# Optimization experiments

Hardware: AMD Instinct MI355X
Metric: run time of the kernel (lower is better)

Reference implementation:

```python
import jax, jax.numpy as jnp
import numpy as np

SAMPLES = 1024
LAM = 0.00051
IOR = 1.515
T_PROP = 8.74
CA = 0.9
LENSLET_CA = 0.165
RMIN = 5.5 * (IOR - 1.0)
RMAX = 29.0 * (IOR - 1.0)
NZ = 10
NLENS = 29
TAU = 30.0
LSE_P = 0.01
PS = 3.6 / SAMPLES
K = 2.0 * np.pi / LAM


def _grids():
    xg = np.linspace(-1.8, 1.8, SAMPLES).astype(np.float32)
    xgm, ygm = np.meshgrid(xg, xg)
    fx = np.linspace(-1.0 / (2.0 * PS), 1.0 / (2.0 * PS), SAMPLES).astype(np.float32)
    Fx, Fy = np.meshgrid(fx, fx)
    return xgm, ygm, Fx, Fy


def _bessj1(x):
    # Numerical Recipes rational approximation of J1 (numpy, setup-time only)
    ax = np.abs(x)
    y = x * x
    p1 = x * (72362614232.0 + y * (-7895059235.0 + y * (242396853.1 + y * (-2972611.439 + y * (15704.48260 + y * (-30.16036606))))))
    q1 = 144725228442.0 + y * (2300535178.0 + y * (18583304.74 + y * (99447.43394 + y * (376.9991397 + y))))
    small = p1 / q1
    axs = np.maximum(ax, 1e-12)
    z = 8.0 / axs
    y2 = z * z
    xx = axs - 2.356194491
    p2 = 1.0 + y2 * (0.183105e-2 + y2 * (-0.3516396496e-4 + y2 * (0.2457520174e-5 + y2 * (-0.240337019e-6))))
    q2 = 0.04687499995 + y2 * (-0.2002690873e-3 + y2 * (0.8449199096e-5 + y2 * (-0.88228987e-6 + y2 * 0.105787412e-6)))
    big = np.sqrt(0.636619772 / axs) * (np.cos(xx) * p2 - z * np.sin(xx) * q2) * np.sign(x)
    return np.where(ax < 8.0, small, big)


def _target_and_mask():
    xgm, ygm, _, _ = _grids()
    target_res = 0.005 * 6  # target_res * M
    D = 1.22 * LAM / np.sin(2.0 * np.arctan(target_res / (2.0 * T_PROP)))
    xa = K * D * np.sin(np.arctan(xgm / T_PROP)) / 2.0
    ya = K * D * np.sin(np.arctan(ygm / T_PROP)) / 2.0
    Ra = np.sqrt(xa * xa + ya * ya)
    ta = (2.0 * _bessj1(Ra) / Ra) ** 2
    ta = ta / np.sqrt(np.sum(ta ** 2))
    tF = np.abs(np.fft.fft2(np.fft.fftshift(ta))) ** 2
    dcm = np.ones_like(tF)
    dcm[:3, :3] = 0; dcm[-2:, :1] = 0; dcm[:1, -2:] = 0; dcm[-2:, -2:] = 0
    dc_mask = ((dcm * tF) > 1e-3 * tF.max()).astype(np.float32)
    return tF.astype(np.float32), dc_mask


def setup_inputs() -> dict:
    rng = np.random.default_rng(0)
    rlist = rng.permutation(1.0 / np.linspace(1.0 / RMAX, 1.0 / RMIN, NLENS)).astype(np.float32)
    th = rng.uniform(0.0, 2.0 * np.pi, NLENS)
    rad = (CA - LENSLET_CA) * np.sqrt(rng.uniform(0.0, 1.0, NLENS))
    xpos = (rad * np.cos(th)).astype(np.float32)
    ypos = (rad * np.sin(th)).astype(np.float32)
    zmin_v = 1.0 / (1.0 / T_PROP - 1.0 / 5.5)
    zmax_v = 1.0 / (1.0 / T_PROP - 1.0 / 29.0)
    defocus = (1.0 / np.linspace(1.0 / zmin_v, 1.0 / zmax_v, NZ)).astype(np.float32)
    tF, dc_mask = _target_and_mask()
    return {
        'rlist': jnp.asarray(rlist), 'xpos': jnp.asarray(xpos), 'ypos': jnp.asarray(ypos),
        'defocus_list': jnp.asarray(defocus),
        'target_F': jnp.asarray(tF), 'dc_mask': jnp.asarray(dc_mask),
    }


def reference(rlist, xpos, ypos, defocus_list, target_F, dc_mask):
    xgm_np, ygm_np, Fx_np, Fy_np = _grids()
    xgm, ygm = jnp.asarray(xgm_np), jnp.asarray(ygm_np)
    Fx, Fy = jnp.asarray(Fx_np), jnp.asarray(Fy_np)

    # ---- lenslet surface synthesis (irregular per-lenslet scatter) ----
    dx2 = (xgm[None] - xpos[:, None, None]) ** 2 + (ygm[None] - ypos[:, None, None]) ** 2  # [N,H,W]
    in_lens = dx2 <= LENSLET_CA ** 2
    r = rlist[:, None, None]
    r2_safe = jnp.where(in_lens, dx2, 0.0)  # avoid nan grads outside lenslet
    sag = r - jnp.sqrt(jnp.maximum(r * r - r2_safe, 1e-12))  # plano-convex sag
    Tsurf = jnp.sum(jnp.where(in_lens, sag, 0.0), axis=0)  # [H,W]
    aper = ((jnp.sum(in_lens.astype(jnp.float32), axis=0) > 0) & (xgm ** 2 + ygm ** 2 <= CA ** 2)).astype(jnp.float32)
    phi_lens = (K * (IOR - 1.0)) * Tsurf

    # ---- angular-spectrum propagation kernel over distance t ----
    kz = jnp.sqrt(jnp.maximum((1.0 / LAM) ** 2 - Fx ** 2 - Fy ** 2, 0.0))
    H = jnp.fft.ifftshift(jnp.exp(1j * (2.0 * np.pi * T_PROP) * kz))

    def psf_one(z):
        phi_in = K * (xgm ** 2 + ygm ** 2) / (2.0 * z)  # paraxial defocus from virtual plane z
        U1 = aper * jnp.exp(1j * (phi_in + phi_lens))
        U2 = jnp.fft.ifft2(jnp.fft.fft2(U1) * H)
        p = jnp.abs(U2) ** 2
        return p / jnp.sum(p)  # l1 psf normalization

    zstack = jax.vmap(psf_one)(defocus_list)  # [Nz,H,W]

    # ---- stack spectrum ----
    S = jnp.fft.fft2(jnp.fft.fftshift(zstack, axes=(-2, -1)))  # [Nz,H,W] complex
    normsize = float(SAMPLES * SAMPLES)

    # diagonal terms: |S|^2 vs target autocorrelation spectrum, dc-masked
    diag = jnp.sum(dc_mask[None] * jnp.square((jnp.abs(S) ** 2 - target_F[None]) / normsize), axis=(-2, -1))  # [Nz]

    # off-diagonal terms: log-sum-exp of |cross-correlation|
    i1, i2 = np.triu_indices(NZ, k=1)  # 45 fixed pairs
    Fcorr = jnp.conj(S[i1]) * S[i2]  # [45,H,W]
    ccorr = jnp.abs(jnp.fft.ifft2(Fcorr))
    off = (TAU * LSE_P) * jax.scipy.special.logsumexp(ccorr.reshape(len(i1), -1) / LSE_P, axis=-1)  # [45]

    return jnp.concatenate([diag, off], axis=0)  # [55]
```

## Files before the change

kernel.cpp:

```cpp
#include <hip/hip_runtime.h>
#include <math.h>

#define NZ 10
#define NLENS 29
#define NPAIR 45
#define NUNIT 23

static __device__ __forceinline__ float2 cmulf(float2 a, float2 b){
    return make_float2(a.x*b.x - a.y*b.y, a.x*b.y + a.y*b.x);
}
#define SW(i) ((i) ^ (((i)>>5)&31))
#define WB() __builtin_amdgcn_wave_barrier()

static constexpr double PI2   = 6.283185307179586;
static constexpr double KD    = PI2/0.00051;
static constexpr double F0D   = 1.0/(2.0*(3.6/1024.0));
static constexpr double FSTEP = 2.0*F0D/1023.0;
static constexpr double IL2D  = (1.0/0.00051)*(1.0/0.00051);
static constexpr double TPPID = PI2*8.74;

static __device__ __forceinline__ void load_W(float2* W, const float2* Wg, int tid){
    for (int t = tid; t < 1024; t += 256) W[SW(t)] = Wg[t];
}

template<bool INV>
static __device__ __forceinline__ void bf4(const float2 a[4], float2 w1, float2 w2, float2 w3, float2 o[4]){
    if (INV){ w1.y = -w1.y; w2.y = -w2.y; w3.y = -w3.y; }
    float2 a1 = cmulf(a[1], w1), a2 = cmulf(a[2], w2), a3 = cmulf(a[3], w3);
    float2 t0 = make_float2(a[0].x+a2.x, a[0].y+a2.y);
    float2 t1 = make_float2(a[0].x-a2.x, a[0].y-a2.y);
    float2 t2 = make_float2(a1.x+a3.x, a1.y+a3.y);
    float2 t3 = make_float2(a1.x-a3.x, a1.y-a3.y);
    o[0] = make_float2(t0.x+t2.x, t0.y+t2.y);
    o[2] = make_float2(t0.x-t2.x, t0.y-t2.y);
    if (!INV){
        o[1] = make_float2(t1.x + t3.y, t1.y - t3.x);
        o[3] = make_float2(t1.x - t3.y, t1.y + t3.x);
    } else {
        o[1] = make_float2(t1.x - t3.y, t1.y + t3.x);
        o[3] = make_float2(t1.x + t3.y, t1.y - t3.x);
    }
}
template<bool INV>
static __device__ __forceinline__ void bf4nt(const float2 a[4], float2 o[4]){
    float2 t0 = make_float2(a[0].x+a[2].x, a[0].y+a[2].y);
    float2 t1 = make_float2(a[0].x-a[2].x, a[0].y-a[2].y);
    float2 t2 = make_float2(a[1].x+a[3].x, a[1].y+a[3].y);
    float2 t3 = make_float2(a[1].x-a[3].x, a[1].y-a[3].y);
    o[0] = make_float2(t0.x+t2.x, t0.y+t2.y);
    o[2] = make_float2(t0.x-t2.x, t0.y-t2.y);
    if (!INV){
        o[1] = make_float2(t1.x + t3.y, t1.y - t3.x);
        o[3] = make_float2(t1.x - t3.y, t1.y + t3.x);
    } else {
        o[1] = make_float2(t1.x - t3.y, t1.y + t3.x);
        o[3] = make_float2(t1.x + t3.y, t1.y - t3.x);
    }
}

static __device__ __forceinline__ void r16_load(const float2* B, int t, float2 a[4][4]){
    #pragma unroll
    for (int k = 0; k < 4; ++k)
        #pragma unroll
        for (int q = 0; q < 4; ++q)
            a[k][q] = B[SW(t + 64*k + 256*q)];
}
template<bool INV>
static __device__ __forceinline__ void r16_s14(const float2 a[4][4], const float2* W, float2 z[4][4]){
    float2 y[4][4];
    #pragma unroll
    for (int k = 0; k < 4; ++k) bf4nt<INV>(a[k], y[k]);
    #pragma unroll
    for (int i = 0; i < 4; ++i){
        float2 b[4] = { y[0][i], y[1][i], y[2][i], y[3][i] };
        bf4<INV>(b, W[SW(64*i)], W[SW(128*i)], W[SW(192*i)], z[i]);
    }
}
static __device__ __forceinline__ void r16_st1(float2* B, int t, const float2 z[4][4]){
    #pragma unroll
    for (int i = 0; i < 4; ++i)
        #pragma unroll
        for (int d = 0; d < 4; ++d)
            B[SW(16*t + i + 4*d)] = z[i][d];
}
template<bool INV>
static __device__ __forceinline__ void r16_s16_64(const float2 a[4][4], const float2* W, int t, float2 z[4][4]){
    int mt = t & 15;
    float2 y[4][4];
    float2 w1 = W[SW(16*mt)], w2 = W[SW(32*mt)], w3 = W[SW(48*mt)];
    #pragma unroll
    for (int k = 0; k < 4; ++k) bf4<INV>(a[k], w1, w2, w3, y[k]);
    #pragma unroll
    for (int n = 0; n < 4; ++n){
        int m2 = mt + 16*n;
        float2 b[4] = { y[0][n], y[1][n], y[2][n], y[3][n] };
        bf4<INV>(b, W[SW(4*m2)], W[SW(8*m2)], W[SW(12*m2)], z[n]);
    }
}
static __device__ __forceinline__ void r16_st2(float2* B, int t, const float2 z[4][4]){
    int base = 256*(t>>4) + (t&15);
    #pragma unroll
    for (int n = 0; n < 4; ++n)
        #pragma unroll
        for (int d = 0; d < 4; ++d)
            B[SW(base + 16*n + 64*d)] = z[n][d];
}
template<bool INV>
static __device__ __forceinline__ void r16_s256(const float2 a[4][4], const float2* W, int t, float2 z[4][4]){
    #pragma unroll
    for (int k = 0; k < 4; ++k){
        int j = t + 64*k;
        bf4<INV>(a[k], W[SW(j)], W[SW(2*j)], W[SW(3*j)], z[k]);
    }
}
static __device__ __forceinline__ void r16_st3(float2* B, int t, const float2 z[4][4]){
    #pragma unroll
    for (int k = 0; k < 4; ++k)
        #pragma unroll
        for (int d = 0; d < 4; ++d)
            B[SW(t + 64*k + 256*d)] = z[k][d];
}
template<bool INV>
static __device__ void r16_fft_regs(float2* B, const float2* W, int t, float2 a[4][4], float2 z[4][4]){
    float2 b[4][4];
    r16_s14<INV>(a, W, z);
    WB(); r16_st1(B, t, z); WB();
    r16_load(B, t, b); r16_s16_64<INV>(b, W, t, z);
    WB(); r16_st2(B, t, z); WB();
    r16_load(B, t, b); r16_s256<INV>(b, W, t, z);
}
template<bool INV>
static __device__ void r16_fft_lds(float2* B, const float2* W, int t, float2 z[4][4]){
    float2 a[4][4];
    r16_load(B, t, a);
    r16_fft_regs<INV>(B, W, t, a, z);
}

static __device__ __forceinline__ float2 expi_from_double(double ph){
    double t = ph * (1.0/PI2);
    t -= floor(t);
    float th = (float)(t * PI2);
    float s, c; sincosf(th, &s, &c);
    return make_float2(c, s);
}

__global__ __launch_bounds__(256) void k_prep(const float* __restrict__ rlist,
        const float* __restrict__ xpos, const float* __restrict__ ypos,
        const float* __restrict__ tF, const float* __restrict__ dm,
        float2* __restrict__ phiA, float2* __restrict__ HT,
        float2* __restrict__ TM, float2* __restrict__ Wg){
    __shared__ float2 T[32][33];
    int b = blockIdx.x, tid = threadIdx.x;
    if (b < 4096){
        int idx = b*256 + tid;
        int r = idx >> 10, c = idx & 1023;
        float x = (float)(-1.8 + c*(3.6/1023.0));
        float y = (float)(-1.8 + r*(3.6/1023.0));
        const float ca2 = (float)(0.165*0.165);
        float Ts = 0.f; int any = 0;
        for (int l = 0; l < NLENS; ++l){
            float dx = x - xpos[l], dy = y - ypos[l];
            float d2 = dx*dx + dy*dy;
            if (d2 <= ca2){
                float rr = rlist[l];
                Ts += rr - sqrtf(fmaxf(rr*rr - d2, 1e-12f));
                any = 1;
            }
        }
        float ap = (any && (x*x + y*y) <= 0.81f) ? 1.f : 0.f;
        float phi = (float)(KD*(1.515 - 1.0)) * Ts;
        phiA[idx] = make_float2(phi, ap);
    } else if (b < 8192){
        int idx = (b-4096)*256 + tid;
        int c = idx >> 10, r = idx & 1023;
        int cs = (c + 512) & 1023, rs = (r + 512) & 1023;
        float fc = (float)(-F0D + cs*FSTEP);
        float fr = (float)(-F0D + rs*FSTEP);
        float kz2 = __fsub_rn(__fsub_rn((float)IL2D, __fmul_rn(fc,fc)), __fmul_rn(fr,fr));
        float kzf = sqrtf(fmaxf(kz2, 0.f));
        float phf = __fmul_rn((float)TPPID, kzf);
        HT[idx] = expi_from_double((double)phf);
    } else if (b < 9216){
        int tb = b - 8192;
        int bx = tb & 31, by = tb >> 5;
        int tx = tid & 31, ty = tid >> 5;
        #pragma unroll
        for (int j = 0; j < 4; ++j){
            int r = by*32 + ty + 8*j, c = bx*32 + tx;
            T[ty+8*j][tx] = make_float2(tF[(size_t)r*1024 + c], dm[(size_t)r*1024 + c]);
        }
        __syncthreads();
        #pragma unroll
        for (int j = 0; j < 4; ++j){
            int c = bx*32 + ty + 8*j, r = by*32 + tx;
            TM[(size_t)c*1024 + r] = T[tx][ty+8*j];
        }
    } else {
        int t = (b-9216)*256 + tid;
        float a = (float)((double)t * (-PI2/1024.0));
        float s, c; sincosf(a, &s, &c);
        Wg[t] = make_float2(c, s);
    }
}

__global__ __launch_bounds__(256) void k_p1(const float2* __restrict__ phiA,
        const float* __restrict__ defocus, float2* __restrict__ S,
        const float2* __restrict__ Wg){
    __shared__ float2 buf[4*1024];
    __shared__ float2 W[1024];
    int tid = threadIdx.x, zz = blockIdx.y;
    load_W(W, Wg, tid);
    __syncthreads();
    int w = tid >> 6, t = tid & 63;
    int row = blockIdx.x*4 + w;
    float2* B = buf + w*1024;
    float zf = defocus[zz];
    float y  = (float)(-1.8 + row*(3.6/1023.0));
    const float KF = (float)KD;
    const float2* pha = phiA + ((size_t)row << 10);
    float2 a[4][4], z[4][4];
    #pragma unroll
    for (int k = 0; k < 4; ++k)
        #pragma unroll
        for (int q = 0; q < 4; ++q){
            int idx = t + 64*k + 256*q;
            float x = (float)(-1.8 + idx*(3.6/1023.0));
            float2 pa = pha[idx];
            float2 u  = make_float2(0.f, 0.f);
            if (pa.y != 0.f){
                float qq     = x*x + y*y;
                float phi_in = (KF*qq) / (2.0f*zf);
                u = expi_from_double((double)(phi_in + pa.x));
            }
            a[k][q] = u;
        }
    r16_fft_regs<false>(B, W, t, a, z);
    float2* Srow = S + ((size_t)zz << 20) + ((size_t)row << 10);
    #pragma unroll
    for (int k = 0; k < 4; ++k)
        #pragma unroll
        for (int d = 0; d < 4; ++d)
            Srow[t + 64*k + 256*d] = z[k][d];
}

__global__ __launch_bounds__(256) void k_p2(float2* __restrict__ S,
        const float2* __restrict__ HT, const float2* __restrict__ Wg){
    __shared__ float2 buf[4*1024];
    __shared__ float2 W[1024];
    int tid = threadIdx.x, bx = blockIdx.x, zz = blockIdx.y;
    int cb = ((bx & 7) << 5) | (bx >> 3);
    int c0 = cb*4;
    load_W(W, Wg, tid);
    float2* Sz = S + ((size_t)zz << 20);
    for (int it = 0; it < 16; ++it){
        int rr = it*64 + (tid>>2), cc = tid & 3;
        buf[cc*1024 + SW(rr)] = Sz[((size_t)rr << 10) + c0 + cc];
    }
    __syncthreads();
    int col = tid >> 6, t = tid & 63;
    float2* B = buf + col*1024;
    float2 z[4][4], a[4][4];
    r16_fft_lds<false>(B, W, t, z);
    const float2* Hc = HT + ((size_t)(c0+col) << 10);
    #pragma unroll
    for (int k = 0; k < 4; ++k)
        #pragma unroll
        for (int d = 0; d < 4; ++d)
            z[k][d] = cmulf(z[k][d], Hc[t + 64*k + 256*d]);
    r16_fft_regs<true>(B, W, t, z, a);
    const float sc = 1.0f/1024.0f;
    #pragma unroll
    for (int k = 0; k < 4; ++k)
        #pragma unroll
        for (int d = 0; d < 4; ++d){ a[k][d].x *= sc; a[k][d].y *= sc; }
    WB();
    r16_st3(B, t, a);
    __syncthreads();
    for (int it = 0; it < 16; ++it){
        int rr = it*64 + (tid>>2), cc = tid & 3;
        Sz[((size_t)rr << 10) + c0 + cc] = buf[cc*1024 + SW(rr)];
    }
}

__global__ __launch_bounds__(256) void k_p3(float2* __restrict__ S,
        float* __restrict__ sumPart, const float2* __restrict__ Wg){
    __shared__ float2 buf[4*1024];
    __shared__ float2 W[1024];
    int tid = threadIdx.x, zz = blockIdx.y;
    load_W(W, Wg, tid);
    __syncthreads();
    int w = tid >> 6, t = tid & 63;
    int row = blockIdx.x*4 + w;
    float2* B = buf + w*1024;
    float2* Srow = S + ((size_t)zz << 20) + ((size_t)row << 10);
    float2 a[4][4], z[4][4];
    #pragma unroll
    for (int k = 0; k < 4; ++k)
        #pragma unroll
        for (int q = 0; q < 4; ++q)
            a[k][q] = Srow[t + 64*k + 256*q];
    r16_fft_regs<true>(B, W, t, a, z);
    const float s2 = (1.0f/1024.0f)*(1.0f/1024.0f);
    float lsum = 0.f;
    #pragma unroll
    for (int k = 0; k < 4; ++k)
        #pragma unroll
        for (int d = 0; d < 4; ++d){
            float2 u = z[k][d];
            float p = (u.x*u.x + u.y*u.y) * s2;
            a[k][d] = make_float2(p, 0.f);
            lsum += p;
        }
    for (int o = 32; o > 0; o >>= 1) lsum += __shfl_down(lsum, o, 64);
    if (t == 0) sumPart[zz*1024 + row] = lsum;
    WB();
    r16_fft_regs<false>(B, W, t, a, z);
    #pragma unroll
    for (int k = 0; k < 4; ++k)
        #pragma unroll
        for (int d = 0; d < 4; ++d)
            Srow[t + 64*k + 256*d] = z[k][d];
}

__global__ __launch_bounds__(256) void k_p4(float2* __restrict__ S,
        const float* __restrict__ sumPart, const float2* __restrict__ TM,
        float* __restrict__ dpart, const float2* __restrict__ Wg){
    __shared__ float2 buf[4*1024];
    __shared__ float2 W[1024];
    int tid = threadIdx.x, bx = blockIdx.x, zz = blockIdx.y;
    int cb = ((bx & 7) << 5) | (bx >> 3);
    int c0 = cb*4;
    load_W(W, Wg, tid);
    float2* Sz = S + ((size_t)zz << 20);
    for (int it = 0; it < 16; ++it){
        int rr = it*64 + (tid>>2), cc = tid & 3;
        buf[cc*1024 + SW(rr)] = Sz[((size_t)rr << 10) + c0 + cc];
    }
    int col = tid >> 6, t = tid & 63;
    double sd = 0.0;
    for (int i = t; i < 1024; i += 64) sd += (double)sumPart[zz*1024 + i];
    for (int o = 32; o > 0; o >>= 1) sd += __shfl_down(sd, o, 64);
    sd = __shfl(sd, 0, 64);
    float inv = (float)(1.0/sd);
    __syncthreads();
    float2* B = buf + col*1024;
    float2 z[4][4];
    r16_fft_lds<false>(B, W, t, z);
    const float2* TMc = TM + ((size_t)(c0+col) << 10);
    const float nrm = 1.0f/1048576.0f;
    float dacc = 0.f;
    #pragma unroll
    for (int k = 0; k < 4; ++k)
        #pragma unroll
        for (int d = 0; d < 4; ++d){
            float2 s = z[k][d]; s.x *= inv; s.y *= inv; z[k][d] = s;
            float2 tm = TMc[t + 64*k + 256*d];
            float dff = (s.x*s.x + s.y*s.y - tm.x) * nrm;
            dacc += tm.y * dff * dff;
        }
    for (int o = 32; o > 0; o >>= 1) dacc += __shfl_down(dacc, o, 64);
    WB();
    r16_st3(B, t, z);
    __syncthreads();
    if (t == 0) ((float*)W)[col] = dacc;
    for (int it = 0; it < 16; ++it){
        int rr = it*64 + (tid>>2), cc = tid & 3;
        Sz[((size_t)rr << 10) + c0 + cc] = buf[cc*1024 + SW(rr)];
    }
    __syncthreads();
    if (tid == 0){
        float* r = (float*)W;
        dpart[zz*256 + cb] = r[0]+r[1]+r[2]+r[3];
    }
}

static __device__ __forceinline__ void pair_of(int p, int& a, int& b){
    int i = 0, c = NZ-1;
    while (p >= c){ p -= c; ++i; --c; }
    a = i; b = i + 1 + p;
}

__global__ __launch_bounds__(256) void k_pairA(const float2* __restrict__ S,
        float2* __restrict__ U, int ubase, const float2* __restrict__ Wg){
    __shared__ float2 buf[4*1024];
    __shared__ float2 W[1024];
    int tid = threadIdx.x, ug = blockIdx.y;
    load_W(W, Wg, tid);
    __syncthreads();
    int w = tid >> 6, t = tid & 63;
    int row = blockIdx.x*4 + w;
    float2* B = buf + w*1024;
    int u = ubase + ug;
    int pa = 2*u, pb = (2*u+1 < NPAIR) ? (2*u+1) : (NPAIR-1);
    int i1, i2, j1, j2;
    pair_of(pa, i1, i2); pair_of(pb, j1, j2);
    const float2* A1 = S + ((size_t)i1 << 20) + ((size_t)row << 10);
    const float2* A2 = S + ((size_t)i2 << 20) + ((size_t)row << 10);
    const float2* B1 = S + ((size_t)j1 << 20) + ((size_t)row << 10);
    const float2* B2 = S + ((size_t)j2 << 20) + ((size_t)row << 10);
    float2 a[4][4], z[4][4];
    #pragma unroll
    for (int k = 0; k < 4; ++k)
        #pragma unroll
        for (int q = 0; q < 4; ++q){
            int idx = t + 64*k + 256*q;
            float2 x1 = A1[idx], y1 = A2[idx], x2 = B1[idx], y2 = B2[idx];
            float2 g1 = make_float2(x1.x*y1.x + x1.y*y1.y, x1.x*y1.y - x1.y*y1.x);
            float2 g2 = make_float2(x2.x*y2.x + x2.y*y2.y, x2.x*y2.y - x2.y*y2.x);
            a[k][q] = make_float2(g1.x - g2.y, g1.y + g2.x);
        }
    r16_fft_regs<true>(B, W, t, a, z);
    const float sc = 1.0f/1024.0f;
    float2* Up = U + ((size_t)ug << 20) + ((size_t)row << 10);
    #pragma unroll
    for (int k = 0; k < 4; ++k)
        #pragma unroll
        for (int d = 0; d < 4; ++d){
            float2 v = z[k][d];
            Up[t + 64*k + 256*d] = make_float2(v.x*sc, v.y*sc);
        }
}

__global__ __launch_bounds__(256) void k_pairB(const float2* __restrict__ U,
        float2* __restrict__ lsePart, int ubase, const float2* __restrict__ Wg){
    __shared__ float2 buf[4*1024];
    __shared__ float2 W[1024];
    int tid = threadIdx.x, bx = blockIdx.x, ug = blockIdx.y;
    int cb = ((bx & 7) << 5) | (bx >> 3);
    int c0 = cb*4;
    int u = ubase + ug;
    load_W(W, Wg, tid);
    const float2* Up = U + ((size_t)ug << 20);
    for (int it = 0; it < 16; ++it){
        int rr = it*64 + (tid>>2), cc = tid & 3;
        buf[cc*1024 + SW(rr)] = Up[((size_t)rr << 10) + c0 + cc];
    }
    __syncthreads();
    int col = tid >> 6, t = tid & 63;
    float2* B = buf + col*1024;
    float2 z[4][4];
    r16_fft_lds<true>(B, W, t, z);
    const float sc = 1.0f/1024.0f;
    float m1 = -1.f, m2 = -1.f;
    #pragma unroll
    for (int k = 0; k < 4; ++k)
        #pragma unroll
        for (int d = 0; d < 4; ++d){
            float c1 = fabsf(z[k][d].x)*sc, c2 = fabsf(z[k][d].y)*sc;
            z[k][d] = make_float2(c1, c2);
            m1 = fmaxf(m1, c1); m2 = fmaxf(m2, c2);
        }
    for (int o = 32; o > 0; o >>= 1){
        m1 = fmaxf(m1, __shfl_down(m1, o, 64));
        m2 = fmaxf(m2, __shfl_down(m2, o, 64));
    }
    if (t == 0) B[0] = make_float2(m1, m2);
    __syncthreads();
    float M1 = -1.f, M2 = -1.f;
    #pragma unroll
    for (int ww = 0; ww < 4; ++ww){
        float2 v = buf[ww*1024];
        M1 = fmaxf(M1, v.x); M2 = fmaxf(M2, v.y);
    }
    float s1 = 0.f, s2 = 0.f;
    #pragma unroll
    for (int k = 0; k < 4; ++k)
        #pragma unroll
        for (int d = 0; d < 4; ++d){
            s1 += expf((z[k][d].x - M1) * 100.0f);
            s2 += expf((z[k][d].y - M2) * 100.0f);
        }
    for (int o = 32; o > 0; o >>= 1){
        s1 += __shfl_down(s1, o, 64);
        s2 += __shfl_down(s2, o, 64);
    }
    if (t == 0) B[1] = make_float2(s1, s2);
    __syncthreads();
    if (tid == 0){
        float S1 = 0.f, S2 = 0.f;
        #pragma unroll
        for (int ww = 0; ww < 4; ++ww){
            float2 v = buf[ww*1024 + 1];
            S1 += v.x; S2 += v.y;
        }
        lsePart[(size_t)(2*u)*256 + cb] = make_float2(M1, S1);
        if (2*u+1 < NPAIR)
            lsePart[(size_t)(2*u+1)*256 + cb] = make_float2(M2, S2);
    }
}

__global__ __launch_bounds__(256) void k_final(const float* __restrict__ dpart,
        const float2* __restrict__ lsePart, float* __restrict__ out){
    __shared__ double dred[4];
    __shared__ float fred[4];
    int b = blockIdx.x, tid = threadIdx.x;
    if (b < NZ){
        double s = (double)dpart[b*256 + tid];
        for (int o = 32; o > 0; o >>= 1) s += __shfl_down(s, o, 64);
        if ((tid & 63) == 0) dred[tid >> 6] = s;
        __syncthreads();
        if (tid == 0) out[b] = (float)(dred[0]+dred[1]+dred[2]+dred[3]);
    } else {
        int p = b - NZ;
        float2 v = lsePart[(size_t)p*256 + tid];
        float m = v.x;
        for (int o = 32; o > 0; o >>= 1) m = fmaxf(m, __shfl_down(m, o, 64));
        if ((tid & 63) == 0) fred[tid >> 6] = m;
        __syncthreads();
        float M = fmaxf(fmaxf(fred[0], fred[1]), fmaxf(fred[2], fred[3]));
        double s = (double)v.y * (double)expf((v.x - M)*100.0f);
        for (int o = 32; o > 0; o >>= 1) s += __shfl_down(s, o, 64);
        if ((tid & 63) == 0) dred[tid >> 6] = s;
        __syncthreads();
        if (tid == 0)
            out[NZ + p] = (float)(30.0*(double)M + 0.3*log(dred[0]+dred[1]+dred[2]+dred[3]));
    }
}

extern "C" void kernel_launch(void* const* d_in, const int* in_sizes, int n_in,
                              void* d_out, int out_size, void* d_ws, size_t ws_size,
                              hipStream_t stream){
    const float* rlist   = (const float*)d_in[0];
    const float* xpos    = (const float*)d_in[1];
    const float* ypos    = (const float*)d_in[2];
    const float* defocus = (const float*)d_in[3];
    const float* tF      = (const float*)d_in[4];
    const float* dmask   = (const float*)d_in[5];
    float* out = (float*)d_out;

    char* ws = (char*)d_ws;
    const size_t S_B = 83886080ull;
    float2* S       = (float2*)(ws);
    char*   tail    = ws + S_B;
    float*  sumPart = (float*) (tail);
    float*  dpart   = (float*) (tail + 65536);
    float2* lsePart = (float2*)(tail + 131072);
    float2* Wg      = (float2*)(tail + 229376);
    char*   X       = ws + S_B + 262144;
    float2* phiA    = (float2*)(X);
    float2* HT      = (float2*)(X + 8388608);
    float2* TM      = (float2*)(X + 16777216);
    float2* U       = (float2*)(X);

    size_t Xoff = S_B + 262144;
    int UB = (ws_size >= Xoff + (64ull<<20)) ? 8 : 6;

    k_prep<<<9220, 256, 0, stream>>>(rlist, xpos, ypos, tF, dmask, phiA, HT, TM, Wg);
    k_p1 <<<dim3(256, NZ), 256, 0, stream>>>(phiA, defocus, S, Wg);
    k_p2 <<<dim3(256, NZ), 256, 0, stream>>>(S, HT, Wg);
    k_p3 <<<dim3(256, NZ), 256, 0, stream>>>(S, sumPart, Wg);
    k_p4 <<<dim3(256, NZ), 256, 0, stream>>>(S, sumPart, TM, dpart, Wg);
    for (int g = 0; g < NUNIT; g += UB){
        int cnt = (NUNIT - g < UB) ? (NUNIT - g) : UB;
        k_pairA<<<dim3(256, cnt), 256, 0, stream>>>(S, U, g, Wg);
        k_pairB<<<dim3(256, cnt), 256, 0, stream>>>(U, lsePart, g, Wg);
    }
    k_final<<<NZ + NPAIR, 256, 0, stream>>>(dpart, lsePart, out);
}
```

Baseline: 525.4 us.

## Transpose FFT intermediates via LDS exchange, exploit Hermitian symmetry, compute H inline

Each row-FFT pass now writes its output transposed, via a padded LDS buffer and float4 stores, so the following column pass reads contiguous rows. The strided column gathers and scatters go away. The real-valued PSF spectrum is kept only for half the columns (513), and pair cross-spectra are rebuilt from the mirrored half, cutting storage and the column-FFT work. The transfer function H is computed inline instead of read from a precomputed table. Aperture and DC-mask data are packed into single floats with a sentinel, z-planes are processed in two batches, and block-level syncs are replaced with per-wave reductions. Costs include extra index arithmetic, recomputed sincos for H, and more kernel launches.

```diff
diff --git a/kernel.cpp b/kernel.cpp
--- a/kernel.cpp
+++ b/kernel.cpp
@@ -5,6 +5,9 @@
 #define NLENS 29
 #define NPAIR 45
 #define NUNIT 23
+#define UB 5
+#define SSTR 1028
+#define PSTH 525312
 
 static __device__ __forceinline__ float2 cmulf(float2 a, float2 b){
     return make_float2(a.x*b.x - a.y*b.y, a.x*b.y + a.y*b.x);
@@ -19,8 +22,9 @@
 static constexpr double IL2D  = (1.0/0.00051)*(1.0/0.00051);
 static constexpr double TPPID = PI2*8.74;
 
-static __device__ __forceinline__ void load_W(float2* W, const float2* Wg, int tid){
-    for (int t = tid; t < 1024; t += 256) W[SW(t)] = Wg[t];
+static __device__ __forceinline__ void load_W_wave(float2* W, const float2* Wg, int t){
+    #pragma unroll
+    for (int i = 0; i < 12; ++i){ int idx = t + 64*i; W[SW(idx)] = Wg[idx]; }
 }
 
 template<bool INV>
@@ -129,12 +133,6 @@
     WB(); r16_st2(B, t, z); WB();
     r16_load(B, t, b); r16_s256<INV>(b, W, t, z);
 }
-template<bool INV>
-static __device__ void r16_fft_lds(float2* B, const float2* W, int t, float2 z[4][4]){
-    float2 a[4][4];
-    r16_load(B, t, a);
-    r16_fft_regs<INV>(B, W, t, a, z);
-}
 
 static __device__ __forceinline__ float2 expi_from_double(double ph){
     double t = ph * (1.0/PI2);
@@ -144,12 +142,28 @@
     return make_float2(c, s);
 }
 
+static __device__ __forceinline__ void exch_write(const float2* buf, float2* dst,
+        int tid, int r0, int jmax){
+    #pragma unroll
+    for (int cc = 0; cc < 4; ++cc){
+        int j = tid + 256*cc;
+        if (j < jmax){
+            float2 v0 = buf[SW(j)];
+            float2 v1 = buf[SSTR + SW(j)];
+            float2 v2 = buf[2*SSTR + SW(j)];
+            float2 v3 = buf[3*SSTR + SW(j)];
+            float4* p = (float4*)(dst + (size_t)j*1024 + r0);
+            p[0] = make_float4(v0.x, v0.y, v1.x, v1.y);
+            p[1] = make_float4(v2.x, v2.y, v3.x, v3.y);
+        }
+    }
+}
+
 __global__ __launch_bounds__(256) void k_prep(const float* __restrict__ rlist,
         const float* __restrict__ xpos, const float* __restrict__ ypos,
         const float* __restrict__ tF, const float* __restrict__ dm,
-        float2* __restrict__ phiA, float2* __restrict__ HT,
-        float2* __restrict__ TM, float2* __restrict__ Wg){
-    __shared__ float2 T[32][33];
+        float* __restrict__ phiA, float* __restrict__ TMv, float2* __restrict__ Wg){
+    __shared__ float Tt[32][33];
     int b = blockIdx.x, tid = threadIdx.x;
     if (b < 4096){
         int idx = b*256 + tid;
@@ -167,57 +181,48 @@
                 any = 1;
             }
         }
-        float ap = (any && (x*x + y*y) <= 0.81f) ? 1.f : 0.f;
+        int ap = any && (x*x + y*y) <= 0.81f;
         float phi = (float)(KD*(1.515 - 1.0)) * Ts;
-        phiA[idx] = make_float2(phi, ap);
-    } else if (b < 8192){
-        int idx = (b-4096)*256 + tid;
-        int c = idx >> 10, r = idx & 1023;
-        int cs = (c + 512) & 1023, rs = (r + 512) & 1023;
-        float fc = (float)(-F0D + cs*FSTEP);
-        float fr = (float)(-F0D + rs*FSTEP);
-        float kz2 = __fsub_rn(__fsub_rn((float)IL2D, __fmul_rn(fc,fc)), __fmul_rn(fr,fr));
-        float kzf = sqrtf(fmaxf(kz2, 0.f));
-        float phf = __fmul_rn((float)TPPID, kzf);
-        HT[idx] = expi_from_double((double)phf);
-    } else if (b < 9216){
-        int tb = b - 8192;
+        phiA[idx] = ap ? phi : -1.0f;
+    } else if (b < 5120){
+        int tb = b - 4096;
         int bx = tb & 31, by = tb >> 5;
         int tx = tid & 31, ty = tid >> 5;
         #pragma unroll
         for (int j = 0; j < 4; ++j){
             int r = by*32 + ty + 8*j, c = bx*32 + tx;
-            T[ty+8*j][tx] = make_float2(tF[(size_t)r*1024 + c], dm[(size_t)r*1024 + c]);
+            float tv = tF[(size_t)r*1024 + c];
+            float mv = dm[(size_t)r*1024 + c];
+            Tt[ty+8*j][tx] = (mv > 0.f) ? tv : -1.0f;
         }
         __syncthreads();
         #pragma unroll
         for (int j = 0; j < 4; ++j){
             int c = bx*32 + ty + 8*j, r = by*32 + tx;
-            TM[(size_t)c*1024 + r] = T[tx][ty+8*j];
+            if (c <= 512) TMv[(size_t)c*1024 + r] = Tt[tx][ty+8*j];
         }
     } else {
-        int t = (b-9216)*256 + tid;
+        int t = (b-5120)*256 + tid;
         float a = (float)((double)t * (-PI2/1024.0));
         float s, c; sincosf(a, &s, &c);
         Wg[t] = make_float2(c, s);
     }
 }
 
-__global__ __launch_bounds__(256) void k_p1(const float2* __restrict__ phiA,
-        const float* __restrict__ defocus, float2* __restrict__ S,
-        const float2* __restrict__ Wg){
-    __shared__ float2 buf[4*1024];
-    __shared__ float2 W[1024];
+__global__ __launch_bounds__(256,4) void k_p1(const float* __restrict__ phiA,
+        const float* __restrict__ defocus, float2* __restrict__ T,
+        const float2* __restrict__ Wg, int zoff){
+    __shared__ float2 buf[4*SSTR];
+    __shared__ float2 W[768];
     int tid = threadIdx.x, zz = blockIdx.y;
-    load_W(W, Wg, tid);
-    __syncthreads();
     int w = tid >> 6, t = tid & 63;
-    int row = blockIdx.x*4 + w;
-    float2* B = buf + w*1024;
-    float zf = defocus[zz];
+    load_W_wave(W, Wg, t);
+    int r0 = blockIdx.x*4, row = r0 + w;
+    float2* B = buf + w*SSTR;
+    float zf = defocus[zoff + zz];
     float y  = (float)(-1.8 + row*(3.6/1023.0));
     const float KF = (float)KD;
-    const float2* pha = phiA + ((size_t)row << 10);
+    const float* pha = phiA + ((size_t)row << 10);
     float2 a[4][4], z[4][4];
     #pragma unroll
     for (int k = 0; k < 4; ++k)
@@ -225,74 +230,75 @@
         for (int q = 0; q < 4; ++q){
             int idx = t + 64*k + 256*q;
             float x = (float)(-1.8 + idx*(3.6/1023.0));
-            float2 pa = pha[idx];
-            float2 u  = make_float2(0.f, 0.f);
-            if (pa.y != 0.f){
-                float qq     = x*x + y*y;
+            float v = pha[idx];
+            float2 uu = make_float2(0.f, 0.f);
+            if (v >= 0.f){
+                float qq = x*x + y*y;
                 float phi_in = (KF*qq) / (2.0f*zf);
-                u = expi_from_double((double)(phi_in + pa.x));
+                uu = expi_from_double((double)(phi_in + v));
             }
-            a[k][q] = u;
+            a[k][q] = uu;
         }
     r16_fft_regs<false>(B, W, t, a, z);
-    float2* Srow = S + ((size_t)zz << 20) + ((size_t)row << 10);
-    #pragma unroll
-    for (int k = 0; k < 4; ++k)
-        #pragma unroll
-        for (int d = 0; d < 4; ++d)
-            Srow[t + 64*k + 256*d] = z[k][d];
-}
-
-__global__ __launch_bounds__(256) void k_p2(float2* __restrict__ S,
-        const float2* __restrict__ HT, const float2* __restrict__ Wg){
-    __shared__ float2 buf[4*1024];
-    __shared__ float2 W[1024];
-    int tid = threadIdx.x, bx = blockIdx.x, zz = blockIdx.y;
-    int cb = ((bx & 7) << 5) | (bx >> 3);
-    int c0 = cb*4;
-    load_W(W, Wg, tid);
-    float2* Sz = S + ((size_t)zz << 20);
-    for (int it = 0; it < 16; ++it){
-        int rr = it*64 + (tid>>2), cc = tid & 3;
-        buf[cc*1024 + SW(rr)] = Sz[((size_t)rr << 10) + c0 + cc];
-    }
+    WB(); r16_st3(B, t, z);
     __syncthreads();
-    int col = tid >> 6, t = tid & 63;
-    float2* B = buf + col*1024;
-    float2 z[4][4], a[4][4];
-    r16_fft_lds<false>(B, W, t, z);
-    const float2* Hc = HT + ((size_t)(c0+col) << 10);
-    #pragma unroll
-    for (int k = 0; k < 4; ++k)
-        #pragma unroll
-        for (int d = 0; d < 4; ++d)
-            z[k][d] = cmulf(z[k][d], Hc[t + 64*k + 256*d]);
+    exch_write(buf, T + ((size_t)zz << 20), tid, r0, 1024);
+}
+
+__global__ __launch_bounds__(256,4) void k_p2(const float2* __restrict__ T,
+        float2* __restrict__ S, const float2* __restrict__ Wg){
+    __shared__ float2 buf[4*SSTR];
+    __shared__ float2 W[768];
+    int tid = threadIdx.x, zz = blockIdx.y;
+    int w = tid >> 6, t = tid & 63;
+    load_W_wave(W, Wg, t);
+    int c0 = blockIdx.x*4, kc = c0 + w;
+    float2* B = buf + w*SSTR;
+    const float2* Tr = T + ((size_t)zz << 20) + ((size_t)kc << 10);
+    float2 a[4][4], z[4][4];
+    #pragma unroll
+    for (int k = 0; k < 4; ++k)
+        #pragma unroll
+        for (int q = 0; q < 4; ++q)
+            a[k][q] = Tr[t + 64*k + 256*q];
+    r16_fft_regs<false>(B, W, t, a, z);
+    int cs = (kc + 512) & 1023;
+    float fc  = (float)(-F0D + cs*FSTEP);
+    float fc2 = __fmul_rn(fc, fc);
+    const float il2f = (float)IL2D, pf = (float)TPPID;
+    #pragma unroll
+    for (int k = 0; k < 4; ++k)
+        #pragma unroll
+        for (int d = 0; d < 4; ++d){
+            int j2 = t + 64*k + 256*d;
+            int rs = (j2 + 512) & 1023;
+            float fr  = (float)(-F0D + rs*FSTEP);
+            float kz2 = __fsub_rn(__fsub_rn(il2f, fc2), __fmul_rn(fr, fr));
+            float kzf = sqrtf(fmaxf(kz2, 0.f));
+            float2 h  = expi_from_double((double)__fmul_rn(pf, kzf));
+            z[k][d] = cmulf(z[k][d], h);
+        }
     r16_fft_regs<true>(B, W, t, z, a);
     const float sc = 1.0f/1024.0f;
     #pragma unroll
     for (int k = 0; k < 4; ++k)
         #pragma unroll
         for (int d = 0; d < 4; ++d){ a[k][d].x *= sc; a[k][d].y *= sc; }
-    WB();
-    r16_st3(B, t, a);
+    WB(); r16_st3(B, t, a);
     __syncthreads();
-    for (int it = 0; it < 16; ++it){
-        int rr = it*64 + (tid>>2), cc = tid & 3;
-        Sz[((size_t)rr << 10) + c0 + cc] = buf[cc*1024 + SW(rr)];
-    }
-}
-
-__global__ __launch_bounds__(256) void k_p3(float2* __restrict__ S,
-        float* __restrict__ sumPart, const float2* __restrict__ Wg){
-    __shared__ float2 buf[4*1024];
-    __shared__ float2 W[1024];
+    exch_write(buf, S + ((size_t)zz << 20), tid, c0, 1024);
+}
+
+__global__ __launch_bounds__(256,4) void k_p3(const float2* __restrict__ S,
+        float2* __restrict__ T2, float* __restrict__ sumPartz, const float2* __restrict__ Wg){
+    __shared__ float2 buf[4*SSTR];
+    __shared__ float2 W[768];
     int tid = threadIdx.x, zz = blockIdx.y;
-    load_W(W, Wg, tid);
-    __syncthreads();
     int w = tid >> 6, t = tid & 63;
-    int row = blockIdx.x*4 + w;
-    float2* B = buf + w*1024;
-    float2* Srow = S + ((size_t)zz << 20) + ((size_t)row << 10);
+    load_W_wave(W, Wg, t);
+    int y0 = blockIdx.x*4, y = y0 + w;
+    float2* B = buf + w*SSTR;
+    const float2* Srow = S + ((size_t)zz << 20) + ((size_t)y << 10);
     float2 a[4][4], z[4][4];
     #pragma unroll
     for (int k = 0; k < 4; ++k)
@@ -312,66 +318,58 @@
             lsum += p;
         }
     for (int o = 32; o > 0; o >>= 1) lsum += __shfl_down(lsum, o, 64);
-    if (t == 0) sumPart[zz*1024 + row] = lsum;
+    if (t == 0) sumPartz[zz*1024 + y] = lsum;
     WB();
     r16_fft_regs<false>(B, W, t, a, z);
-    #pragma unroll
-    for (int k = 0; k < 4; ++k)
-        #pragma unroll
-        for (int d = 0; d < 4; ++d)
-            Srow[t + 64*k + 256*d] = z[k][d];
-}
-
-__global__ __launch_bounds__(256) void k_p4(float2* __restrict__ S,
-        const float* __restrict__ sumPart, const float2* __restrict__ TM,
-        float* __restrict__ dpart, const float2* __restrict__ Wg){
-    __shared__ float2 buf[4*1024];
-    __shared__ float2 W[1024];
-    int tid = threadIdx.x, bx = blockIdx.x, zz = blockIdx.y;
-    int cb = ((bx & 7) << 5) | (bx >> 3);
-    int c0 = cb*4;
-    load_W(W, Wg, tid);
-    float2* Sz = S + ((size_t)zz << 20);
-    for (int it = 0; it < 16; ++it){
-        int rr = it*64 + (tid>>2), cc = tid & 3;
-        buf[cc*1024 + SW(rr)] = Sz[((size_t)rr << 10) + c0 + cc];
-    }
-    int col = tid >> 6, t = tid & 63;
+    WB(); r16_st3(B, t, z);
+    __syncthreads();
+    exch_write(buf, T2 + (size_t)zz*PSTH, tid, y0, 513);
+}
+
+__global__ __launch_bounds__(256,4) void k_p4(const float2* __restrict__ T2,
+        float2* __restrict__ ST, const float* __restrict__ sumPartz,
+        const float* __restrict__ TMv, float* __restrict__ dpartz,
+        const float2* __restrict__ Wg){
+    __shared__ float2 buf[4*SSTR];
+    __shared__ float2 W[768];
+    int tid = threadIdx.x, zz = blockIdx.y;
+    int w = tid >> 6, t = tid & 63;
+    int kc = blockIdx.x*4 + w;
+    if (kc > 512) return;
+    load_W_wave(W, Wg, t);
+    float2* B = buf + w*SSTR;
     double sd = 0.0;
-    for (int i = t; i < 1024; i += 64) sd += (double)sumPart[zz*1024 + i];
+    for (int i = t; i < 1024; i += 64) sd += (double)sumPartz[zz*1024 + i];
     for (int o = 32; o > 0; o >>= 1) sd += __shfl_down(sd, o, 64);
     sd = __shfl(sd, 0, 64);
     float inv = (float)(1.0/sd);
-    __syncthreads();
-    float2* B = buf + col*1024;
-    float2 z[4][4];
-    r16_fft_lds<false>(B, W, t, z);
-    const float2* TMc = TM + ((size_t)(c0+col) << 10);
+    const float2* Tr = T2 + (size_t)zz*PSTH + ((size_t)kc << 10);
+    float2 a[4][4], z[4][4];
+    #pragma unroll
+    for (int k = 0; k < 4; ++k)
+        #pragma unroll
+        for (int q = 0; q < 4; ++q)
+            a[k][q] = Tr[t + 64*k + 256*q];
+    r16_fft_regs<false>(B, W, t, a, z);
+    const float* TMc = TMv + ((size_t)kc << 10);
     const float nrm = 1.0f/1048576.0f;
     float dacc = 0.f;
+    float2* STr = ST + (size_t)zz*PSTH + ((size_t)kc << 10);
     #pragma unroll
     for (int k = 0; k < 4; ++k)
         #pragma unroll
         for (int d = 0; d < 4; ++d){
-            float2 s = z[k][d]; s.x *= inv; s.y *= inv; z[k][d] = s;
-            float2 tm = TMc[t + 64*k + 256*d];
-            float dff = (s.x*s.x + s.y*s.y - tm.x) * nrm;
-            dacc += tm.y * dff * dff;
+            float2 s = z[k][d]; s.x *= inv; s.y *= inv;
+            float tmv = TMc[t + 64*k + 256*d];
+            if (tmv >= 0.f){
+                float dff = (s.x*s.x + s.y*s.y - tmv) * nrm;
+                dacc += dff * dff;
+            }
+            STr[t + 64*k + 256*d] = s;
         }
     for (int o = 32; o > 0; o >>= 1) dacc += __shfl_down(dacc, o, 64);
-    WB();
-    r16_st3(B, t, z);
-    __syncthreads();
-    if (t == 0) ((float*)W)[col] = dacc;
-    for (int it = 0; it < 16; ++it){
-        int rr = it*64 + (tid>>2), cc = tid & 3;
-        Sz[((size_t)rr << 10) + c0 + cc] = buf[cc*1024 + SW(rr)];
-    }
-    __syncthreads();
-    if (tid == 0){
-        float* r = (float*)W;
-        dpart[zz*256 + cb] = r[0]+r[1]+r[2]+r[3];
-    }
+    float wgt = (kc == 0 || kc == 512) ? 1.f : 2.f;
+    if (t == 0) dpartz[zz*1024 + kc] = dacc * wgt;
 }
 
 static __device__ __forceinline__ void pair_of(int p, int& a, int& b){
@@ -380,66 +378,70 @@
     a = i; b = i + 1 + p;
 }
 
-__global__ __launch_bounds__(256) void k_pairA(const float2* __restrict__ S,
+__global__ __launch_bounds__(256,4) void k_pairA(const float2* __restrict__ ST,
         float2* __restrict__ U, int ubase, const float2* __restrict__ Wg){
-    __shared__ float2 buf[4*1024];
-    __shared__ float2 W[1024];
+    __shared__ float2 buf[4*SSTR];
+    __shared__ float2 W[768];
     int tid = threadIdx.x, ug = blockIdx.y;
-    load_W(W, Wg, tid);
-    __syncthreads();
     int w = tid >> 6, t = tid & 63;
-    int row = blockIdx.x*4 + w;
-    float2* B = buf + w*1024;
+    load_W_wave(W, Wg, t);
+    int c0 = blockIdx.x*4, kc = c0 + w;
+    float2* B = buf + w*SSTR;
     int u = ubase + ug;
     int pa = 2*u, pb = (2*u+1 < NPAIR) ? (2*u+1) : (NPAIR-1);
     int i1, i2, j1, j2;
     pair_of(pa, i1, i2); pair_of(pb, j1, j2);
-    const float2* A1 = S + ((size_t)i1 << 20) + ((size_t)row << 10);
-    const float2* A2 = S + ((size_t)i2 << 20) + ((size_t)row << 10);
-    const float2* B1 = S + ((size_t)j1 << 20) + ((size_t)row << 10);
-    const float2* B2 = S + ((size_t)j2 << 20) + ((size_t)row << 10);
+    int mirror = (kc > 512);
+    int kci = mirror ? (1024 - kc) : kc;
+    const float2* P1 = ST + (size_t)i1*PSTH + ((size_t)kci << 10);
+    const float2* Q1 = ST + (size_t)i2*PSTH + ((size_t)kci << 10);
+    const float2* P2 = ST + (size_t)j1*PSTH + ((size_t)kci << 10);
+    const float2* Q2 = ST + (size_t)j2*PSTH + ((size_t)kci << 10);
+    if (mirror){
+        const float2* tmp = P1; P1 = Q1; Q1 = tmp;
+        tmp = P2; P2 = Q2; Q2 = tmp;
+    }
     float2 a[4][4], z[4][4];
     #pragma unroll
     for (int k = 0; k < 4; ++k)
         #pragma unroll
         for (int q = 0; q < 4; ++q){
             int idx = t + 64*k + 256*q;
-            float2 x1 = A1[idx], y1 = A2[idx], x2 = B1[idx], y2 = B2[idx];
+            int ix  = mirror ? ((1024 - idx) & 1023) : idx;
+            float2 x1 = P1[ix], y1 = Q1[ix], x2 = P2[ix], y2 = Q2[ix];
             float2 g1 = make_float2(x1.x*y1.x + x1.y*y1.y, x1.x*y1.y - x1.y*y1.x);
             float2 g2 = make_float2(x2.x*y2.x + x2.y*y2.y, x2.x*y2.y - x2.y*y2.x);
             a[k][q] = make_float2(g1.x - g2.y, g1.y + g2.x);
         }
     r16_fft_regs<true>(B, W, t, a, z);
     const float sc = 1.0f/1024.0f;
-    float2* Up = U + ((size_t)ug << 20) + ((size_t)row << 10);
-    #pragma unroll
-    for (int k = 0; k < 4; ++k)
-        #pragma unroll
-        for (int d = 0; d < 4; ++d){
-            float2 v = z[k][d];
-            Up[t + 64*k + 256*d] = make_float2(v.x*sc, v.y*sc);
-        }
-}
-
-__global__ __launch_bounds__(256) void k_pairB(const float2* __restrict__ U,
+    #pragma unroll
+    for (int k = 0; k < 4; ++k)
+        #pragma unroll
+        for (int d = 0; d < 4; ++d){ z[k][d].x *= sc; z[k][d].y *= sc; }
+    WB(); r16_st3(B, t, z);
+    __syncthreads();
+    exch_write(buf, U + ((size_t)ug << 20), tid, c0, 1024);
+}
+
+__global__ __launch_bounds__(256,4) void k_pairB(const float2* __restrict__ U,
         float2* __restrict__ lsePart, int ubase, const float2* __restrict__ Wg){
-    __shared__ float2 buf[4*1024];
-    __shared__ float2 W[1024];
-    int tid = threadIdx.x, bx = blockIdx.x, ug = blockIdx.y;
-    int cb = ((bx & 7) << 5) | (bx >> 3);
-    int c0 = cb*4;
+    __shared__ float2 buf[4*SSTR];
+    __shared__ float2 W[768];
+    int tid = threadIdx.x, ug = blockIdx.y;
+    int w = tid >> 6, t = tid & 63;
+    load_W_wave(W, Wg, t);
+    int y = blockIdx.x*4 + w;
+    float2* B = buf + w*SSTR;
     int u = ubase + ug;
-    load_W(W, Wg, tid);
-    const float2* Up = U + ((size_t)ug << 20);
-    for (int it = 0; it < 16; ++it){
-        int rr = it*64 + (tid>>2), cc = tid & 3;
-        buf[cc*1024 + SW(rr)] = Up[((size_t)rr << 10) + c0 + cc];
-    }
-    __syncthreads();
-    int col = tid >> 6, t = tid & 63;
-    float2* B = buf + col*1024;
-    float2 z[4][4];
-    r16_fft_lds<true>(B, W, t, z);
+    const float2* Urow = U + ((size_t)ug << 20) + ((size_t)y << 10);
+    float2 a[4][4], z[4][4];
+    #pragma unroll
+    for (int k = 0; k < 4; ++k)
+        #pragma unroll
+        for (int q = 0; q < 4; ++q)
+            a[k][q] = Urow[t + 64*k + 256*q];
+    r16_fft_regs<true>(B, W, t, a, z);
     const float sc = 1.0f/1024.0f;
     float m1 = -1.f, m2 = -1.f;
     #pragma unroll
@@ -454,14 +456,7 @@
         m1 = fmaxf(m1, __shfl_down(m1, o, 64));
         m2 = fmaxf(m2, __shfl_down(m2, o, 64));
     }
-    if (t == 0) B[0] = make_float2(m1, m2);
-    __syncthreads();
-    float M1 = -1.f, M2 = -1.f;
-    #pragma unroll
-    for (int ww = 0; ww < 4; ++ww){
-        float2 v = buf[ww*1024];
-        M1 = fmaxf(M1, v.x); M2 = fmaxf(M2, v.y);
-    }
+    float M1 = __shfl(m1, 0, 64), M2 = __shfl(m2, 0, 64);
     float s1 = 0.f, s2 = 0.f;
     #pragma unroll
     for (int k = 0; k < 4; ++k)
@@ -474,18 +469,10 @@
         s1 += __shfl_down(s1, o, 64);
         s2 += __shfl_down(s2, o, 64);
     }
-    if (t == 0) B[1] = make_float2(s1, s2);
-    __syncthreads();
-    if (tid == 0){
-        float S1 = 0.f, S2 = 0.f;
-        #pragma unroll
-        for (int ww = 0; ww < 4; ++ww){
-            float2 v = buf[ww*1024 + 1];
-            S1 += v.x; S2 += v.y;
-        }
-        lsePart[(size_t)(2*u)*256 + cb] = make_float2(M1, S1);
+    if (t == 0){
+        lsePart[(size_t)(2*u)*1024 + y] = make_float2(M1, s1);
         if (2*u+1 < NPAIR)
-            lsePart[(size_t)(2*u+1)*256 + cb] = make_float2(M2, S2);
+            lsePart[(size_t)(2*u+1)*1024 + y] = make_float2(M2, s2);
     }
 }
 
@@ -495,20 +482,26 @@
     __shared__ float fred[4];
     int b = blockIdx.x, tid = threadIdx.x;
     if (b < NZ){
-        double s = (double)dpart[b*256 + tid];
+        double s = (double)dpart[b*1024 + tid] + (double)dpart[b*1024 + 256 + tid];
+        if (tid == 0) s += (double)dpart[b*1024 + 512];
         for (int o = 32; o > 0; o >>= 1) s += __shfl_down(s, o, 64);
         if ((tid & 63) == 0) dred[tid >> 6] = s;
         __syncthreads();
         if (tid == 0) out[b] = (float)(dred[0]+dred[1]+dred[2]+dred[3]);
     } else {
         int p = b - NZ;
-        float2 v = lsePart[(size_t)p*256 + tid];
-        float m = v.x;
+        const float2* lp = lsePart + (size_t)p*1024;
+        float2 v[4]; float m = -1e30f;
+        #pragma unroll
+        for (int c = 0; c < 4; ++c){ v[c] = lp[tid + 256*c]; m = fmaxf(m, v[c].x); }
         for (int o = 32; o > 0; o >>= 1) m = fmaxf(m, __shfl_down(m, o, 64));
         if ((tid & 63) == 0) fred[tid >> 6] = m;
         __syncthreads();
         float M = fmaxf(fmaxf(fred[0], fred[1]), fmaxf(fred[2], fred[3]));
-        double s = (double)v.y * (double)expf((v.x - M)*100.0f);
+        double s = 0.0;
+        #pragma unroll
+        for (int c = 0; c < 4; ++c)
+            s += (double)v[c].y * (double)expf((v[c].x - M)*100.0f);
         for (int o = 32; o > 0; o >>= 1) s += __shfl_down(s, o, 64);
         if ((tid & 63) == 0) dred[tid >> 6] = s;
         __syncthreads();
@@ -529,31 +522,30 @@
     float* out = (float*)d_out;
 
     char* ws = (char*)d_ws;
-    const size_t S_B = 83886080ull;
-    float2* S       = (float2*)(ws);
-    char*   tail    = ws + S_B;
+    float2* ST   = (float2*)(ws);
+    float2* Sbat = (float2*)(ws + 42024960);
+    float2* A    = (float2*)(ws + 83968000);
+    float*  phiA = (float*) (ws + 125911040);
+    float*  TMv  = (float*) (ws + 130105344);
+    char*   tail = ws + 132206592;
     float*  sumPart = (float*) (tail);
-    float*  dpart   = (float*) (tail + 65536);
-    float2* lsePart = (float2*)(tail + 131072);
-    float2* Wg      = (float2*)(tail + 229376);
-    char*   X       = ws + S_B + 262144;
-    float2* phiA    = (float2*)(X);
-    float2* HT      = (float2*)(X + 8388608);
-    float2* TM      = (float2*)(X + 16777216);
-    float2* U       = (float2*)(X);
-
-    size_t Xoff = S_B + 262144;
-    int UB = (ws_size >= Xoff + (64ull<<20)) ? 8 : 6;
-
-    k_prep<<<9220, 256, 0, stream>>>(rlist, xpos, ypos, tF, dmask, phiA, HT, TM, Wg);
-    k_p1 <<<dim3(256, NZ), 256, 0, stream>>>(phiA, defocus, S, Wg);
-    k_p2 <<<dim3(256, NZ), 256, 0, stream>>>(S, HT, Wg);
-    k_p3 <<<dim3(256, NZ), 256, 0, stream>>>(S, sumPart, Wg);
-    k_p4 <<<dim3(256, NZ), 256, 0, stream>>>(S, sumPart, TM, dpart, Wg);
+    float*  dpart   = (float*) (tail + 40960);
+    float2* lsePart = (float2*)(tail + 81920);
+    float2* Wg      = (float2*)(tail + 450560);
+
+    k_prep<<<5123, 256, 0, stream>>>(rlist, xpos, ypos, tF, dmask, phiA, TMv, Wg);
+    for (int bz = 0; bz < 2; ++bz){
+        int zoff = bz*5;
+        k_p1<<<dim3(256, 5), 256, 0, stream>>>(phiA, defocus, A, Wg, zoff);
+        k_p2<<<dim3(256, 5), 256, 0, stream>>>(A, Sbat, Wg);
+        k_p3<<<dim3(256, 5), 256, 0, stream>>>(Sbat, A, sumPart + zoff*1024, Wg);
+        k_p4<<<dim3(129, 5), 256, 0, stream>>>(A, ST + (size_t)zoff*PSTH,
+                sumPart + zoff*1024, TMv, dpart + zoff*1024, Wg);
+    }
     for (int g = 0; g < NUNIT; g += UB){
         int cnt = (NUNIT - g < UB) ? (NUNIT - g) : UB;
-        k_pairA<<<dim3(256, cnt), 256, 0, stream>>>(S, U, g, Wg);
-        k_pairB<<<dim3(256, cnt), 256, 0, stream>>>(U, lsePart, g, Wg);
+        k_pairA<<<dim3(256, cnt), 256, 0, stream>>>(ST, (float2*)A, g, Wg);
+        k_pairB<<<dim3(256, cnt), 256, 0, stream>>>((float2*)A, lsePart, g, Wg);
     }
     k_final<<<NZ + NPAIR, 256, 0, stream>>>(dpart, lsePart, out);
 }
```

Result: slower. 688.8 us (+31.1%).
